# Kernel optimization log

Measured on AMD Instinct MI355X. Metric: run time of the kernel, lower is better.

## Reference

```python
import jax, jax.numpy as jnp
import numpy as np

TABLE_SIZE = 256
I16_MIN, I16_MAX = -32768.0, 32767.0
I8_MIN, I8_MAX = -128.0, 127.0
MAX_SOFTMAX_VALUE = 1.0
OUT_SCALE = MAX_SOFTMAX_VALUE * 2.0 / 255.0            # int8 output scale
EXP_OUT_SCALE = 2.0 / 65535.0                          # qint16 exp output scale
RECIP_OUT_SCALE = (1.0 / 0.1) * 2.0 / 65535.0          # qint16 reciprocal output scale
# (xmin, xmax, kind) in ascending x order; 'table' = 256-entry LUT, 'line' = linear fit
EXP_REGIONS = [(-40.0, -20.0, 'line'), (-20.0, -10.0, 'table'), (-10.0, 0.0, 'table'), (0.0, 1.0, 'line')]
RECIP_REGIONS = [(0.001, 0.1, 'line'), (0.1, 250.0, 'table'), (250.0, 500.0, 'table'), (500.0, 700.0, 'line')]


def _quant(y, out_scale, qmin, qmax):
    return jnp.clip(jnp.round(y / out_scale), qmin, qmax)


def _piecewise(x, func, regions, out_scale, qmin, qmax):
    """Piecewise quantized approximation of func: constant / line / 256-entry
    table regions, returning quantized (integer-valued float) outputs."""
    left_c = _quant(func(jnp.float32(regions[0][0])), out_scale, qmin, qmax)
    y = left_c * jnp.ones_like(x)
    for xmin, xmax, kind in regions:
        if kind == 'table':
            xs = jnp.linspace(xmin, xmax, TABLE_SIZE)
            tab = _quant(func(xs), out_scale, qmin, qmax)
            idx = jnp.clip(jnp.round((x - xmin) * ((TABLE_SIZE - 1) / (xmax - xmin))), 0, TABLE_SIZE - 1).astype(jnp.int32)
            y_r = tab[idx]
        else:
            y0 = func(jnp.float32(xmin))
            y1 = func(jnp.float32(xmax))
            y_r = _quant(y0 + (x - xmin) * ((y1 - y0) / (xmax - xmin)), out_scale, qmin, qmax)
        y = jnp.where(x >= xmin, y_r, y)
    right_c = _quant(func(jnp.float32(regions[-1][1])), out_scale, qmin, qmax)
    return jnp.where(x > regions[-1][1], right_c, y)


def setup_inputs() -> dict:
    key = jax.random.key(0)
    k1, _ = jax.random.split(key)
    data = jax.random.randint(k1, (32, 128, 80, 80), -128, 128, dtype=jnp.int32)  # int8 repr, zp=0
    data_scale = jnp.array([0.0625], dtype=jnp.float32)
    return {"data": data, "data_scale": data_scale}


def reference(data, data_scale):
    ds = data_scale[0]
    C = data.shape[1]
    shift = float(np.ceil(np.log2(C)))  # rescale_shift for the exp-sum
    # max-subtract in the integer domain, dequantize diff (zero_point = 0)
    qmax = jnp.max(data, axis=1, keepdims=True)
    xd = (data - qmax).astype(jnp.float32) * ds  # [B,C,H,W], in (-inf, 0]
    # quantized exp via piecewise tables -> qint16 with EXP_OUT_SCALE
    exp_q = _piecewise(xd, jnp.exp, EXP_REGIONS, EXP_OUT_SCALE, I16_MIN, I16_MAX)
    # sum over channels, right-shift back into int16 range
    sum_q = jnp.sum(exp_q, axis=1, keepdims=True)
    sum_sh = jnp.clip(jnp.round(sum_q * (2.0 ** -shift)), I16_MIN, I16_MAX)
    div_scale = EXP_OUT_SCALE * (2.0 ** shift)  # div_data_scale
    # quantized reciprocal of the (dequantized) shifted sum -> qint16
    recip_q = _piecewise(sum_sh * div_scale, lambda v: 1.0 / v, RECIP_REGIONS, RECIP_OUT_SCALE, I16_MIN, I16_MAX)
    # out = exp * recip, requantized to int8 with OUT_SCALE, then dequantized
    out_q = jnp.clip(jnp.round(exp_q * recip_q * (EXP_OUT_SCALE * RECIP_OUT_SCALE / OUT_SCALE)), I8_MIN, I8_MAX)
    return out_q * OUT_SCALE
```

## Files before the change

### kernel.cpp

```cpp
#include <hip/hip_runtime.h>
#include <cmath>

#define NB  32
#define NC  128
#define NHW 6400
#define PIX 64
#define TPB 256


__global__ __launch_bounds__(TPB) void qsoftmax_kernel(
    const int* __restrict__ data,
    const float* __restrict__ dscale,
    float* __restrict__ out) {
#pragma clang fp contract(off)
  __shared__ int   exp_tab[256];
  __shared__ float recip_tab[256];
  __shared__ int4  red[16][16];
  __shared__ int4  qmax_s[16];
  __shared__ float4 rq_s[16];

  const int t  = threadIdx.x;
  const int k  = t >> 4;
  const int p4 = t & 15;

  const int blk  = blockIdx.x;
  const int b    = blk / (NHW / PIX);
  const int hw0  = (blk % (NHW / PIX)) * PIX;
  const int base4 = b * NC * (NHW / 4) + (hw0 >> 2);

  const float ds = dscale[0];

  {
    const float EXP_SCALE_F = (float)(2.0 / 65535.0);
    float x = (float)(-t) * ds;
    float e;
    if (x >= 0.0f) {
      float y0 = expf(0.0f), y1 = expf(1.0f);
      e = rintf((y0 + x * ((y1 - y0) / 1.0f)) / EXP_SCALE_F);
    } else if (x >= -10.0f) {
      float delta = 10.0f / 255.0f;
      float idxf = rintf((x + 10.0f) * 25.5f);
      idxf = fminf(fmaxf(idxf, 0.0f), 255.0f);
      float xs = -10.0f + idxf * delta;
      e = rintf((float)exp((double)xs) / EXP_SCALE_F);
    } else {
      float delta = 10.0f / 255.0f;
      float idxf = rintf((x + 20.0f) * 25.5f);
      idxf = fminf(fmaxf(idxf, 0.0f), 255.0f);
      float xs = -20.0f + idxf * delta;
      e = rintf((float)exp((double)xs) / EXP_SCALE_F);
    }
    e = fminf(fmaxf(e, -32768.0f), 32767.0f);
    exp_tab[t] = (int)e;

    const float RECIP_SCALE_F = (float)((1.0 / 0.1) * 2.0 / 65535.0);
    float deltar = (250.0f - 0.1f) / 255.0f;
    float xs = 0.1f + (float)t * deltar;
    float r = rintf((1.0f / xs) / RECIP_SCALE_F);
    r = fminf(fmaxf(r, -32768.0f), 32767.0f);
    recip_tab[t] = r;
  }

  int4 d[8];
  const int4* g4 = (const int4*)data;
#pragma unroll
  for (int i = 0; i < 8; ++i) {
    d[i] = g4[base4 + (16 * i + k) * (NHW / 4) + p4];
  }

  int4 m = d[0];
#pragma unroll
  for (int i = 1; i < 8; ++i) {
    m.x = max(m.x, d[i].x); m.y = max(m.y, d[i].y);
    m.z = max(m.z, d[i].z); m.w = max(m.w, d[i].w);
  }
  red[k][p4] = m;
  __syncthreads();
  if (k == 0) {
    int4 q = red[0][p4];
#pragma unroll
    for (int kk = 1; kk < 16; ++kk) {
      int4 r = red[kk][p4];
      q.x = max(q.x, r.x); q.y = max(q.y, r.y);
      q.z = max(q.z, r.z); q.w = max(q.w, r.w);
    }
    qmax_s[p4] = q;
  }
  __syncthreads();

  const int4 q = qmax_s[p4];
  int4 s = make_int4(0, 0, 0, 0);
#pragma unroll
  for (int i = 0; i < 8; ++i) {
    int4 v = d[i];
    int e0 = exp_tab[min(q.x - v.x, 255)];
    int e1 = exp_tab[min(q.y - v.y, 255)];
    int e2 = exp_tab[min(q.z - v.z, 255)];
    int e3 = exp_tab[min(q.w - v.w, 255)];
    s.x += e0; s.y += e1; s.z += e2; s.w += e3;
    d[i] = make_int4(e0, e1, e2, e3);
  }
  red[k][p4] = s;
  __syncthreads();
  if (k == 0) {
    int4 tot = red[0][p4];
#pragma unroll
    for (int kk = 1; kk < 16; ++kk) {
      int4 r = red[kk][p4];
      tot.x += r.x; tot.y += r.y; tot.z += r.z; tot.w += r.w;
    }
    const float DIV_SCALE_F = (float)((2.0 / 65535.0) * 128.0);
    const float RIDX_K_F    = (float)(255.0 / (250.0 - 0.1));
    auto recip_of = [&](int total) -> float {
      float ss = rintf((float)total * 0.0078125f);
      ss = fminf(fmaxf(ss, -32768.0f), 32767.0f);
      float v = ss * DIV_SCALE_F;
      float idxf = rintf((v - 0.1f) * RIDX_K_F);
      idxf = fminf(fmaxf(idxf, 0.0f), 255.0f);
      return recip_tab[(int)idxf];
    };
    float4 rq;
    rq.x = recip_of(tot.x);
    rq.y = recip_of(tot.y);
    rq.z = recip_of(tot.z);
    rq.w = recip_of(tot.w);
    rq_s[p4] = rq;
  }
  __syncthreads();

  const float4 rq = rq_s[p4];
  const float K_F = (float)((2.0 / 65535.0) * ((1.0 / 0.1) * 2.0 / 65535.0) / (2.0 / 255.0));
  const float OUT_SCALE_F = (float)(2.0 / 255.0);
  float4* o4 = (float4*)out;
#pragma unroll
  for (int i = 0; i < 8; ++i) {
    float4 o;
    o.x = fminf(fmaxf(rintf(((float)d[i].x * rq.x) * K_F), -128.0f), 127.0f) * OUT_SCALE_F;
    o.y = fminf(fmaxf(rintf(((float)d[i].y * rq.y) * K_F), -128.0f), 127.0f) * OUT_SCALE_F;
    o.z = fminf(fmaxf(rintf(((float)d[i].z * rq.z) * K_F), -128.0f), 127.0f) * OUT_SCALE_F;
    o.w = fminf(fmaxf(rintf(((float)d[i].w * rq.w) * K_F), -128.0f), 127.0f) * OUT_SCALE_F;
    o4[base4 + (16 * i + k) * (NHW / 4) + p4] = o;
  }
}

extern "C" void kernel_launch(void* const* d_in, const int* in_sizes, int n_in,
                              void* d_out, int out_size, void* d_ws, size_t ws_size,
                              hipStream_t stream) {
  const int* data     = (const int*)d_in[0];
  const float* dscale = (const float*)d_in[1];
  float* out          = (float*)d_out;
  (void)in_sizes; (void)n_in; (void)d_ws; (void)ws_size; (void)out_size;

  dim3 grid(NB * (NHW / PIX));
  qsoftmax_kernel<<<grid, TPB, 0, stream>>>(data, dscale, out);
}
```

Measured before the change: 188.6 us.

## Pack int8/int16 values in registers, redundant reductions, drop barriers, nontemporal stores

Input values are packed as four bytes per register and exp results as two 16-bit values per register, which cuts register pressure to allow more waves per CU. Every thread now repeats the cross-channel max and sum reductions from shared memory, so the k==0 serial phases and two barriers go away. Output stores use nontemporal hints to avoid polluting the cache. The packing relies on the inputs being in int8 range and exp values fitting in 16 bits, and the redundant reductions add LDS reads.

```diff
diff --git a/kernel.cpp b/kernel.cpp
--- a/kernel.cpp
+++ b/kernel.cpp
@@ -7,6 +7,8 @@
 #define PIX 64
 #define TPB 256
 
+typedef float vfloat4 __attribute__((ext_vector_type(4)));
+
 
 __global__ __launch_bounds__(TPB) void qsoftmax_kernel(
     const int* __restrict__ data,
@@ -15,9 +17,8 @@
 #pragma clang fp contract(off)
   __shared__ int   exp_tab[256];
   __shared__ float recip_tab[256];
-  __shared__ int4  red[16][16];
-  __shared__ int4  qmax_s[16];
-  __shared__ float4 rq_s[16];
+  __shared__ int4  red_m[16][16];
+  __shared__ int4  red_s[16][16];
 
   const int t  = threadIdx.x;
   const int k  = t >> 4;
@@ -61,85 +62,86 @@
     recip_tab[t] = r;
   }
 
-  int4 d[8];
   const int4* g4 = (const int4*)data;
+  int pd[8];
+  int4 m = make_int4(-128, -128, -128, -128);
 #pragma unroll
   for (int i = 0; i < 8; ++i) {
-    d[i] = g4[base4 + (16 * i + k) * (NHW / 4) + p4];
+    int4 v = g4[base4 + (16 * i + k) * (NHW / 4) + p4];
+    m.x = max(m.x, v.x); m.y = max(m.y, v.y);
+    m.z = max(m.z, v.z); m.w = max(m.w, v.w);
+    pd[i] = (v.x & 255) | ((v.y & 255) << 8) | ((v.z & 255) << 16) |
+            (int)((unsigned)(v.w & 255) << 24);
+  }
+  red_m[k][p4] = m;
+  __syncthreads();
+
+  int4 q = red_m[0][p4];
+#pragma unroll
+  for (int kk = 1; kk < 16; ++kk) {
+    int4 r = red_m[kk][p4];
+    q.x = max(q.x, r.x); q.y = max(q.y, r.y);
+    q.z = max(q.z, r.z); q.w = max(q.w, r.w);
   }
 
-  int4 m = d[0];
-#pragma unroll
-  for (int i = 1; i < 8; ++i) {
-    m.x = max(m.x, d[i].x); m.y = max(m.y, d[i].y);
-    m.z = max(m.z, d[i].z); m.w = max(m.w, d[i].w);
-  }
-  red[k][p4] = m;
-  __syncthreads();
-  if (k == 0) {
-    int4 q = red[0][p4];
-#pragma unroll
-    for (int kk = 1; kk < 16; ++kk) {
-      int4 r = red[kk][p4];
-      q.x = max(q.x, r.x); q.y = max(q.y, r.y);
-      q.z = max(q.z, r.z); q.w = max(q.w, r.w);
-    }
-    qmax_s[p4] = q;
-  }
-  __syncthreads();
-
-  const int4 q = qmax_s[p4];
+  int pe[16];
   int4 s = make_int4(0, 0, 0, 0);
 #pragma unroll
   for (int i = 0; i < 8; ++i) {
-    int4 v = d[i];
-    int e0 = exp_tab[min(q.x - v.x, 255)];
-    int e1 = exp_tab[min(q.y - v.y, 255)];
-    int e2 = exp_tab[min(q.z - v.z, 255)];
-    int e3 = exp_tab[min(q.w - v.w, 255)];
+    int pdv = pd[i];
+    int c0 = (pdv << 24) >> 24;
+    int c1 = (pdv << 16) >> 24;
+    int c2 = (pdv << 8) >> 24;
+    int c3 = pdv >> 24;
+    int e0 = exp_tab[q.x - c0];
+    int e1 = exp_tab[q.y - c1];
+    int e2 = exp_tab[q.z - c2];
+    int e3 = exp_tab[q.w - c3];
     s.x += e0; s.y += e1; s.z += e2; s.w += e3;
-    d[i] = make_int4(e0, e1, e2, e3);
+    pe[2 * i]     = e0 | (e1 << 16);
+    pe[2 * i + 1] = e2 | (e3 << 16);
   }
-  red[k][p4] = s;
+  red_s[k][p4] = s;
   __syncthreads();
-  if (k == 0) {
-    int4 tot = red[0][p4];
+
+  int4 tot = red_s[0][p4];
 #pragma unroll
-    for (int kk = 1; kk < 16; ++kk) {
-      int4 r = red[kk][p4];
-      tot.x += r.x; tot.y += r.y; tot.z += r.z; tot.w += r.w;
-    }
-    const float DIV_SCALE_F = (float)((2.0 / 65535.0) * 128.0);
-    const float RIDX_K_F    = (float)(255.0 / (250.0 - 0.1));
-    auto recip_of = [&](int total) -> float {
-      float ss = rintf((float)total * 0.0078125f);
+  for (int kk = 1; kk < 16; ++kk) {
+    int4 r = red_s[kk][p4];
+    tot.x += r.x; tot.y += r.y; tot.z += r.z; tot.w += r.w;
+  }
+  const float DIV_SCALE_F = (float)((2.0 / 65535.0) * 128.0);
+  const float RIDX_K_F    = (float)(255.0 / (250.0 - 0.1));
+  float rq[4];
+  {
+    int tv[4] = {tot.x, tot.y, tot.z, tot.w};
+#pragma unroll
+    for (int j = 0; j < 4; ++j) {
+      float ss = rintf((float)tv[j] * 0.0078125f);
       ss = fminf(fmaxf(ss, -32768.0f), 32767.0f);
       float v = ss * DIV_SCALE_F;
       float idxf = rintf((v - 0.1f) * RIDX_K_F);
       idxf = fminf(fmaxf(idxf, 0.0f), 255.0f);
-      return recip_tab[(int)idxf];
-    };
-    float4 rq;
-    rq.x = recip_of(tot.x);
-    rq.y = recip_of(tot.y);
-    rq.z = recip_of(tot.z);
-    rq.w = recip_of(tot.w);
-    rq_s[p4] = rq;
+      rq[j] = recip_tab[(int)idxf];
+    }
   }
-  __syncthreads();
 
-  const float4 rq = rq_s[p4];
   const float K_F = (float)((2.0 / 65535.0) * ((1.0 / 0.1) * 2.0 / 65535.0) / (2.0 / 255.0));
   const float OUT_SCALE_F = (float)(2.0 / 255.0);
-  float4* o4 = (float4*)out;
+  vfloat4* o4 = (vfloat4*)out;
 #pragma unroll
   for (int i = 0; i < 8; ++i) {
-    float4 o;
-    o.x = fminf(fmaxf(rintf(((float)d[i].x * rq.x) * K_F), -128.0f), 127.0f) * OUT_SCALE_F;
-    o.y = fminf(fmaxf(rintf(((float)d[i].y * rq.y) * K_F), -128.0f), 127.0f) * OUT_SCALE_F;
-    o.z = fminf(fmaxf(rintf(((float)d[i].z * rq.z) * K_F), -128.0f), 127.0f) * OUT_SCALE_F;
-    o.w = fminf(fmaxf(rintf(((float)d[i].w * rq.w) * K_F), -128.0f), 127.0f) * OUT_SCALE_F;
-    o4[base4 + (16 * i + k) * (NHW / 4) + p4] = o;
+    int pa = pe[2 * i], pb = pe[2 * i + 1];
+    float e0 = (float)(pa & 0xFFFF);
+    float e1 = (float)(pa >> 16);
+    float e2 = (float)(pb & 0xFFFF);
+    float e3 = (float)(pb >> 16);
+    vfloat4 o;
+    o.x = fminf(fmaxf(rintf((e0 * rq[0]) * K_F), -128.0f), 127.0f) * OUT_SCALE_F;
+    o.y = fminf(fmaxf(rintf((e1 * rq[1]) * K_F), -128.0f), 127.0f) * OUT_SCALE_F;
+    o.z = fminf(fmaxf(rintf((e2 * rq[2]) * K_F), -128.0f), 127.0f) * OUT_SCALE_F;
+    o.w = fminf(fmaxf(rintf((e3 * rq[3]) * K_F), -128.0f), 127.0f) * OUT_SCALE_F;
+    __builtin_nontemporal_store(o, &o4[base4 + (16 * i + k) * (NHW / 4) + p4]);
   }
 }
 
```

Result: no change. 187.8 us (-0.4%).
